# Kernel tuning notes

Hardware: AMD Instinct MI355X
Metric: run time of the kernel (lower is better)

## Reference

```python
import jax, jax.numpy as jnp
import numpy as np
from jax import lax

BN_EPS = 1e-5


def ternarize(w):
    """Per-output-channel ternary quantization (Li & Liu TWN style).
    delta_i = 0.7 * mean(|w_i|); alpha_i = mean of |w| over entries with |w| > delta_i;
    output = alpha_i * (+1 where w > delta_i, -1 where w < -delta_i, else 0).
    """
    aw = jnp.abs(w)
    axes = tuple(range(1, w.ndim))
    delta = 0.7 * jnp.mean(aw, axis=axes)            # [O]
    d = delta.reshape((-1,) + (1,) * (w.ndim - 1))   # broadcastable
    mask = aw > d
    alpha = jnp.sum(aw * mask, axis=axes) / jnp.sum(mask, axis=axes)
    tern = jnp.where(w > d, 1.0, 0.0) - jnp.where(w < -d, 1.0, 0.0)
    return tern * alpha.reshape(d.shape)


def batchnorm2d(x, gamma, beta):
    # training-mode batchnorm: batch statistics over (N, H, W), biased variance
    mean = jnp.mean(x, axis=(0, 2, 3), keepdims=True)
    var = jnp.mean((x - mean) ** 2, axis=(0, 2, 3), keepdims=True)
    xhat = (x - mean) * lax.rsqrt(var + BN_EPS)
    return xhat * gamma[None, :, None, None] + beta[None, :, None, None]


def conv2d(x, w, b):
    out = lax.conv_general_dilated(x, w, window_strides=(1, 1), padding='VALID',
                                   dimension_numbers=('NCHW', 'OIHW', 'NCHW'))
    return out + b[None, :, None, None]


def maxpool2(x):
    return lax.reduce_window(x, -jnp.inf, lax.max, (1, 1, 2, 2), (1, 1, 2, 2), 'VALID')


def setup_inputs() -> dict:
    key = jax.random.key(0)
    ks = jax.random.split(key, 10)
    B = 4096
    return {
        'x': jax.random.normal(ks[0], (B, 1, 28, 28), jnp.float32),
        'w_conv1': jax.random.normal(ks[1], (32, 1, 5, 5), jnp.float32) * 0.2,
        'b_conv1': jax.random.normal(ks[2], (32,), jnp.float32) * 0.1,
        'gamma1': jnp.ones((32,), jnp.float32),
        'beta1': jnp.zeros((32,), jnp.float32),
        'w_conv2': jax.random.normal(ks[3], (64, 32, 5, 5), jnp.float32) * 0.05,
        'b_conv2': jax.random.normal(ks[4], (64,), jnp.float32) * 0.1,
        'gamma2': jnp.ones((64,), jnp.float32),
        'beta2': jnp.zeros((64,), jnp.float32),
        'w_fc1': jax.random.normal(ks[5], (512, 1024), jnp.float32) * 0.03,
        'b_fc1': jax.random.normal(ks[6], (512,), jnp.float32) * 0.1,
        'w_fc2': jax.random.normal(ks[7], (10, 512), jnp.float32) * 0.05,
        'b_fc2': jax.random.normal(ks[8], (10,), jnp.float32) * 0.1,
    }


def reference(x, w_conv1, b_conv1, gamma1, beta1, w_conv2, b_conv2, gamma2, beta2,
              w_fc1, b_fc1, w_fc2, b_fc2):
    h = conv2d(x, ternarize(w_conv1), b_conv1)          # [B,32,24,24]
    h = jax.nn.relu(maxpool2(batchnorm2d(h, gamma1, beta1)))  # [B,32,12,12]
    h = conv2d(h, ternarize(w_conv2), b_conv2)          # [B,64,8,8]
    h = jax.nn.relu(maxpool2(batchnorm2d(h, gamma2, beta2)))  # [B,64,4,4]
    h = h.reshape(-1, 1024)
    h = jax.nn.relu(h @ ternarize(w_fc1).T + b_fc1)     # [B,512]
    return h @ ternarize(w_fc2).T + b_fc2               # [B,10]
```

## Files before the change

### kernel.cpp

```cpp
#include <hip/hip_runtime.h>

#define TID ((int)threadIdx.x)
typedef unsigned short ushort_t;
typedef short short8 __attribute__((ext_vector_type(8)));
typedef float f32x4 __attribute__((ext_vector_type(4)));

__device__ __forceinline__ float bf2f(ushort_t u) {
    return __uint_as_float(((unsigned int)u) << 16);
}
__device__ __forceinline__ ushort_t f2bf(float f) {
    unsigned int x = __float_as_uint(f);
    return (ushort_t)((x + 0x7FFFu + ((x >> 16) & 1u)) >> 16);
}
__device__ __forceinline__ float ld1(const void* p, int i, bool f32) {
    return f32 ? ((const float*)p)[i] : bf2f(((const ushort_t*)p)[i]);
}
__device__ __forceinline__ bool probe_f32(const void* g1) {
    return ((const ushort_t*)g1)[0] == 0x0000u;
}

__global__ __launch_bounds__(256) void tern_pack_kernel(
    const void* __restrict__ w1, const void* __restrict__ w2,
    const void* __restrict__ wf1, const void* __restrict__ wf2,
    ushort_t* __restrict__ wpack1, ushort_t* __restrict__ wpack2,
    ushort_t* __restrict__ wf1pack, ushort_t* __restrict__ wf2pack,
    float* __restrict__ stats_z, const void* __restrict__ g1probe)
{
    const bool f32 = probe_f32(g1probe);
    const int blk = blockIdx.x;
    if (blk < 48) stats_z[blk * 256 + TID] = 0.f;

    const void* w; int K, o, seg;
    if (blk < 32)       { w = w1;  K = 25;   o = blk;       seg = 0; }
    else if (blk < 96)  { w = w2;  K = 800;  o = blk - 32;  seg = 1; }
    else if (blk < 608) { w = wf1; K = 1024; o = blk - 96;  seg = 2; }
    else                { w = wf2; K = 512;  o = blk - 608; seg = 3; }

    const size_t base = (size_t)o * K;
    __shared__ float red[256];
    __shared__ float red2[256];

    float s = 0.f;
    for (int k = TID; k < K; k += 256) s += fabsf(ld1(w, base + k, f32));
    red[TID] = s; __syncthreads();
    for (int st = 128; st > 0; st >>= 1) {
        if (TID < st) red[TID] += red[TID + st];
        __syncthreads();
    }
    const float delta = 0.7f * red[0] / (float)K;
    __syncthreads();

    float ms = 0.f, cnt = 0.f;
    for (int k = TID; k < K; k += 256) {
        float aw = fabsf(ld1(w, base + k, f32));
        if (aw > delta) { ms += aw; cnt += 1.f; }
    }
    red[TID] = ms; red2[TID] = cnt; __syncthreads();
    for (int st = 128; st > 0; st >>= 1) {
        if (TID < st) { red[TID] += red[TID + st]; red2[TID] += red2[TID + st]; }
        __syncthreads();
    }
    const float denom = red2[0];
    const float alpha = (denom > 0.f) ? (red[0] / denom) : 0.f;

    for (int k = TID; k < K; k += 256) {
        float v = ld1(w, base + k, f32);
        ushort_t tb = f2bf((v > delta) ? alpha : ((v < -delta) ? -alpha : 0.f));
        if (seg == 0) {
            const int kp = (k / 5) * 6 + (k % 5);
            wpack1[((size_t)(o >> 4) * 64 + (kp >> 3) * 16 + (o & 15)) * 8 + (kp & 7)] = tb;
        } else if (seg == 1) {
            const int pos = k % 25, ic = k / 25;
            wpack2[((size_t)(pos * 4 + (o >> 4)) * 64 + (ic >> 3) * 16 + (o & 15)) * 8
                   + (ic & 7)] = tb;
        } else if (seg == 2) {
            wf1pack[((size_t)((k >> 5) * 32 + (o >> 4)) * 64 + ((k >> 3) & 3) * 16
                     + (o & 15)) * 8 + (k & 7)] = tb;
        } else {
            wf2pack[((size_t)(k >> 5) * 64 + ((k >> 3) & 3) * 16 + o) * 8 + (k & 7)] = tb;
        }
    }
    if (seg == 0 && TID < 7) {
        const int kps[7] = {5, 11, 17, 23, 29, 30, 31};
        const int kp = kps[TID];
        wpack1[((size_t)(o >> 4) * 64 + (kp >> 3) * 16 + (o & 15)) * 8 + (kp & 7)] = 0;
    }
}

__device__ __forceinline__ void conv1_koff(int qd, int* koff) {
#pragma unroll
    for (int j = 0; j < 8; ++j) {
        int k = qd * 8 + j, ky = k / 6, kx = k - ky * 6;
        koff[j] = (k < 30 && kx < 5) ? (ky * 28 + kx) : -1;
    }
}

__global__ __launch_bounds__(256) void conv1_stats_kernel(
    const void* __restrict__ x, const ushort_t* __restrict__ wpack1u,
    const void* __restrict__ gamma1, float* __restrict__ stats,
    ushort_t* __restrict__ pooled1)
{
    const bool f32 = probe_f32(gamma1);
    const short8* wpack1 = (const short8*)wpack1u;
    __shared__ ushort_t xs[2][784];
    __shared__ float reds[4][64];
    const int b0 = blockIdx.x * 2;
    for (int c = TID; c < 392; c += 256) {
        const int img = (c >= 196) ? 1 : 0;
        const int cc = c - img * 196;
        if (f32) {
            float4 v4 = ((const float4*)x)[(size_t)(b0 + img) * 196 + cc];
            ushort4 u;
            u.x = f2bf(v4.x); u.y = f2bf(v4.y); u.z = f2bf(v4.z); u.w = f2bf(v4.w);
            *(ushort4*)&xs[img][cc * 4] = u;
        } else {
            *(ushort4*)&xs[img][cc * 4] =
                ((const ushort4*)x)[(size_t)(b0 + img) * 196 + cc];
        }
    }
    __syncthreads();

    const int lane = TID & 63, wv = TID >> 6;
    const int img = wv >> 1, wvi = wv & 1;
    const int qd = lane >> 4, ln15 = lane & 15;
    int koff[8];
    conv1_koff(qd, koff);
    const short8 bw0 = wpack1[lane];
    const short8 bw1 = wpack1[64 + lane];
    const bool pos0 = ld1(gamma1, ln15, f32) >= 0.f;
    const bool pos1 = ld1(gamma1, 16 + ln15, f32) >= 0.f;

    float s0 = 0.f, q0 = 0.f, s1 = 0.f, q1 = 0.f;
    const int cellA0 = (ln15 >> 2);
    const int m3 = ln15 & 3;
    const size_t pb = (size_t)(b0 + img) * 144;
    const ushort_t* xsi = xs[img];
    for (int t = wvi * 18; t < wvi * 18 + 18; ++t) {
        const int cellA = t * 4 + cellA0;
        const int pbase = ((cellA / 12) * 2 + (m3 >> 1)) * 28
                        + (cellA % 12) * 2 + (m3 & 1);
        short8 a;
#pragma unroll
        for (int j = 0; j < 8; ++j)
            a[j] = (koff[j] >= 0) ? (short)xsi[pbase + koff[j]] : (short)0;
        f32x4 c0 = {0.f, 0.f, 0.f, 0.f}, c1 = {0.f, 0.f, 0.f, 0.f};
        c0 = __builtin_amdgcn_mfma_f32_16x16x32_bf16(a, bw0, c0, 0, 0, 0);
        c1 = __builtin_amdgcn_mfma_f32_16x16x32_bf16(a, bw1, c1, 0, 0, 0);
#pragma unroll
        for (int r = 0; r < 4; ++r) {
            s0 += c0[r]; q0 += c0[r] * c0[r];
            s1 += c1[r]; q1 += c1[r] * c1[r];
        }
        float mx0 = fmaxf(fmaxf(c0[0], c0[1]), fmaxf(c0[2], c0[3]));
        float mn0 = fminf(fminf(c0[0], c0[1]), fminf(c0[2], c0[3]));
        float mx1 = fmaxf(fmaxf(c1[0], c1[1]), fmaxf(c1[2], c1[3]));
        float mn1 = fminf(fminf(c1[0], c1[1]), fminf(c1[2], c1[3]));
        const int cell = t * 4 + qd;
        pooled1[(pb + cell) * 32 + ln15]      = f2bf(pos0 ? mx0 : mn0);
        pooled1[(pb + cell) * 32 + 16 + ln15] = f2bf(pos1 ? mx1 : mn1);
    }
    s0 += __shfl_xor(s0, 16); q0 += __shfl_xor(q0, 16);
    s1 += __shfl_xor(s1, 16); q1 += __shfl_xor(q1, 16);
    s0 += __shfl_xor(s0, 32); q0 += __shfl_xor(q0, 32);
    s1 += __shfl_xor(s1, 32); q1 += __shfl_xor(q1, 32);
    if (lane < 16) {
        reds[wv][ln15]      = s0;
        reds[wv][32 + ln15] = q0;
        reds[wv][16 + ln15] = s1;
        reds[wv][48 + ln15] = q1;
    }
    __syncthreads();
    if (TID < 64) {
        float v = reds[0][TID] + reds[1][TID] + reds[2][TID] + reds[3][TID];
        atomicAdd(&stats[(blockIdx.x & 63) * 64 + TID], v);
    }
}

__global__ __launch_bounds__(256) void conv12_kernel(
    const ushort_t* __restrict__ pooled1, const float* __restrict__ stats,
    const void* __restrict__ gamma1, const void* __restrict__ beta1,
    const ushort_t* __restrict__ wpack2u,
    const void* __restrict__ b2, const void* __restrict__ gamma2,
    ushort_t* __restrict__ pooled2, float* __restrict__ stats2)
{
    const bool f32 = probe_f32(gamma1);
    const short8* wpack2 = (const short8*)wpack2u;
    __shared__ ushort_t p1b[144 * 40];
    __shared__ float r2[4][64];
    __shared__ float bn4[4][64];
    __shared__ float as1[32], hs1[32];
    const int b = blockIdx.x;

    {
        const int c = TID & 63, g = TID >> 6;
        float v = 0.f;
        for (int sl = g; sl < 64; sl += 4) v += stats[sl * 64 + c];
        bn4[g][c] = v;
    }
    __syncthreads();
    if (TID < 32) {
        float s = bn4[0][TID] + bn4[1][TID] + bn4[2][TID] + bn4[3][TID];
        float q = bn4[0][32 + TID] + bn4[1][32 + TID]
                + bn4[2][32 + TID] + bn4[3][32 + TID];
        const float invN = 1.f / 2359296.f;
        float mraw = s * invN;
        float var  = q * invN - mraw * mraw;
        float rstd = rsqrtf(fmaxf(var, 0.f) + 1e-5f);
        float g1v = ld1(gamma1, TID, f32) * rstd;
        as1[TID] = g1v;
        hs1[TID] = ld1(beta1, TID, f32) - mraw * g1v;
    }
    __syncthreads();

    {
        const uint* pm = (const uint*)(pooled1 + (size_t)b * 4608);
        const int ch2 = (TID * 2) & 31;
        const float aA = as1[ch2],     hA = hs1[ch2];
        const float aB = as1[ch2 + 1], hB = hs1[ch2 + 1];
#pragma unroll
        for (int i = 0; i < 9; ++i) {
            const int idx = i * 256 + TID;
            const uint u = pm[idx];
            const int cell = idx >> 4;
            float v0 = bf2f((ushort_t)(u & 0xFFFFu));
            float v1 = bf2f((ushort_t)(u >> 16));
            uint o0 = f2bf(fmaxf(fmaf(aA, v0, hA), 0.f));
            uint o1 = f2bf(fmaxf(fmaf(aB, v1, hB), 0.f));
            *(uint*)&p1b[cell * 40 + ch2] = o0 | (o1 << 16);
        }
    }
    __syncthreads();

    const int lane = TID & 63, wv = TID >> 6;
    const int qd = lane >> 4, ln15 = lane & 15;
    const int mh = wv >> 1, nh = wv & 1;
    const int px0 = (mh * 2 + 0) * 16 + ln15;
    const int px1 = (mh * 2 + 1) * 16 + ln15;
    const int base0 = (px0 >> 3) * 12 + (px0 & 7);
    const int base1 = (px1 >> 3) * 12 + (px1 & 7);

    f32x4 acc[2][2] = {};
#pragma unroll
    for (int pos = 0; pos < 25; ++pos) {
        const int koff2 = (pos / 5) * 12 + (pos % 5);
        short8 a0 = *(const short8*)&p1b[(base0 + koff2) * 40 + qd * 8];
        short8 a1 = *(const short8*)&p1b[(base1 + koff2) * 40 + qd * 8];
        short8 bb0 = wpack2[(pos * 4 + nh * 2 + 0) * 64 + lane];
        short8 bb1 = wpack2[(pos * 4 + nh * 2 + 1) * 64 + lane];
        acc[0][0] = __builtin_amdgcn_mfma_f32_16x16x32_bf16(a0, bb0, acc[0][0], 0, 0, 0);
        acc[0][1] = __builtin_amdgcn_mfma_f32_16x16x32_bf16(a0, bb1, acc[0][1], 0, 0, 0);
        acc[1][0] = __builtin_amdgcn_mfma_f32_16x16x32_bf16(a1, bb0, acc[1][0], 0, 0, 0);
        acc[1][1] = __builtin_amdgcn_mfma_f32_16x16x32_bf16(a1, bb1, acc[1][1], 0, 0, 0);
    }

    const size_t p2base = (size_t)b * 1024;
#pragma unroll
    for (int jn = 0; jn < 2; ++jn) {
        const int oc = (nh * 2 + jn) * 16 + ln15;
        const float bias = ld1(b2, oc, f32);
        const bool gpos = ld1(gamma2, oc, f32) >= 0.f;
        float s0 = 0.f, q0 = 0.f;
#pragma unroll
        for (int i = 0; i < 2; ++i) {
            float v0 = acc[i][jn][0] + bias;
            float v1 = acc[i][jn][1] + bias;
            float v2 = acc[i][jn][2] + bias;
            float v3 = acc[i][jn][3] + bias;
            s0 += v0 + v1 + v2 + v3;
            q0 += v0*v0 + v1*v1 + v2*v2 + v3*v3;
            float mx01 = fmaxf(v0, v1), mn01 = fminf(v0, v1);
            float mx23 = fmaxf(v2, v3), mn23 = fminf(v2, v3);
            mx01 = fmaxf(mx01, __shfl_xor(mx01, 32));
            mn01 = fminf(mn01, __shfl_xor(mn01, 32));
            mx23 = fmaxf(mx23, __shfl_xor(mx23, 32));
            mn23 = fminf(mn23, __shfl_xor(mn23, 32));
            if (qd < 2) {
                ushort2 st;
                st.x = f2bf(gpos ? mx01 : mn01);
                st.y = f2bf(gpos ? mx23 : mn23);
                const int ti = mh * 2 + i;
                *(ushort2*)&pooled2[p2base + (size_t)oc * 16 + ti * 4 + 2 * qd] = st;
            }
        }
        s0 += __shfl_down(s0, 32); q0 += __shfl_down(q0, 32);
        s0 += __shfl_down(s0, 16); q0 += __shfl_down(q0, 16);
        if (lane < 16) {
            r2[wv][jn * 32 + lane]      = s0;
            r2[wv][jn * 32 + 16 + lane] = q0;
        }
    }
    __syncthreads();
    if (TID < 128) {
        const int idx = TID & 63, nh2 = TID >> 6;
        float v = r2[nh2][idx] + r2[nh2 + 2][idx];
        const int jn = idx >> 5, isq = (idx >> 4) & 1, chx = idx & 15;
        const int oc = nh2 * 32 + jn * 16 + chx;
        atomicAdd(&stats2[(blockIdx.x & 63) * 128 + isq * 64 + oc], v);
    }
}

__global__ __launch_bounds__(256) void fc1_kernel(
    const ushort_t* __restrict__ pooled2, const ushort_t* __restrict__ wf1packu,
    const float* __restrict__ stats2,
    const void* __restrict__ gamma2, const void* __restrict__ beta2,
    const void* __restrict__ bias, ushort_t* __restrict__ out,
    const void* __restrict__ g1probe)
{
    const bool f32 = probe_f32(g1probe);
    const short8* wf1pack = (const short8*)wf1packu;
    __shared__ ushort_t As[64 * 136];
    __shared__ float bn2[2][128];
    __shared__ float a2s[64], h2s[64];
    const int m0 = blockIdx.y * 64;
    const int n0x4 = blockIdx.x * 4;
    const int lane = TID & 63;
    const int wv   = TID >> 6;
    const int mh = wv >> 1, nh = wv & 1;
    const int qd = lane >> 4, ln15 = lane & 15;

    {
        const int c = TID & 127, g = TID >> 7;
        float v = 0.f;
        for (int sl = g; sl < 64; sl += 2) v += stats2[sl * 128 + c];
        bn2[g][c] = v;
    }
    __syncthreads();
    if (TID < 64) {
        float s = bn2[0][TID] + bn2[1][TID];
        float q = bn2[0][64 + TID] + bn2[1][64 + TID];
        const float invN = 1.f / 262144.f;
        float mean = s * invN;
        float var  = q * invN - mean * mean;
        float rstd = rsqrtf(fmaxf(var, 0.f) + 1e-5f);
        float g2 = ld1(gamma2, TID, f32) * rstd;
        a2s[TID] = g2;
        h2s[TID] = ld1(beta2, TID, f32) - mean * g2;
    }

    f32x4 acc[2][2] = {};
    for (int stage = 0; stage < 8; ++stage) {
        __syncthreads();
#pragma unroll
        for (int i = 0; i < 4; ++i) {
            const int idx = i * 256 + TID;
            const int row = idx >> 4, ch = idx & 15;
            const int k = stage * 128 + ch * 8;
            const int oc = k >> 4;
            const float a2 = a2s[oc], h2 = h2s[oc];
            uint4 u = *(const uint4*)&pooled2[(size_t)(m0 + row) * 1024 + k];
            uint4 o;
            uint* up = &u.x; uint* op = &o.x;
#pragma unroll
            for (int q = 0; q < 4; ++q) {
                float lo = bf2f((ushort_t)(up[q] & 0xFFFFu));
                float hi = bf2f((ushort_t)(up[q] >> 16));
                uint olo = f2bf(fmaxf(fmaf(a2, lo, h2), 0.f));
                uint ohi = f2bf(fmaxf(fmaf(a2, hi, h2), 0.f));
                op[q] = olo | (ohi << 16);
            }
            *(uint4*)&As[row * 136 + ch * 8] = o;
        }
        __syncthreads();
#pragma unroll
        for (int ks = 0; ks < 4; ++ks) {
            const int kk = stage * 4 + ks;
            const int col = ks * 32 + qd * 8;
            short8 a0 = *(const short8*)&As[(mh * 32 + ln15) * 136 + col];
            short8 a1 = *(const short8*)&As[(mh * 32 + 16 + ln15) * 136 + col];
            short8 bb0 = wf1pack[(kk * 32 + n0x4 + nh * 2 + 0) * 64 + lane];
            short8 bb1 = wf1pack[(kk * 32 + n0x4 + nh * 2 + 1) * 64 + lane];
            acc[0][0] = __builtin_amdgcn_mfma_f32_16x16x32_bf16(a0, bb0, acc[0][0], 0, 0, 0);
            acc[0][1] = __builtin_amdgcn_mfma_f32_16x16x32_bf16(a0, bb1, acc[0][1], 0, 0, 0);
            acc[1][0] = __builtin_amdgcn_mfma_f32_16x16x32_bf16(a1, bb0, acc[1][0], 0, 0, 0);
            acc[1][1] = __builtin_amdgcn_mfma_f32_16x16x32_bf16(a1, bb1, acc[1][1], 0, 0, 0);
        }
    }

#pragma unroll
    for (int jn = 0; jn < 2; ++jn) {
        const int n = n0x4 * 16 + (nh * 2 + jn) * 16 + ln15;
        const float bv = ld1(bias, n, f32);
#pragma unroll
        for (int i = 0; i < 2; ++i) {
            const int mb = m0 + (mh * 2 + i) * 16 + qd * 4;
#pragma unroll
            for (int r = 0; r < 4; ++r) {
                float v = fmaxf(acc[i][jn][r] + bv, 0.f);
                out[(size_t)(mb + r) * 512 + n] = f2bf(v);
            }
        }
    }
}

__global__ __launch_bounds__(256) void fc2_kernel(
    const ushort_t* __restrict__ h, const ushort_t* __restrict__ wf2packu,
    const void* __restrict__ bias, void* __restrict__ out,
    const void* __restrict__ g1probe)
{
    const bool f32 = probe_f32(g1probe);
    const short8* wf2pack = (const short8*)wf2packu;
    const int lane = TID & 63, wv = TID >> 6;
    const int qd = lane >> 4, ln15 = lane & 15;
    const int m0 = (blockIdx.x * 4 + wv) * 16;

    f32x4 acc = {0.f, 0.f, 0.f, 0.f};
#pragma unroll
    for (int kk = 0; kk < 16; ++kk) {
        short8 a = *(const short8*)&h[(size_t)(m0 + ln15) * 512 + kk * 32 + qd * 8];
        acc = __builtin_amdgcn_mfma_f32_16x16x32_bf16(a, wf2pack[kk * 64 + lane],
                                                      acc, 0, 0, 0);
    }
    if (ln15 < 10) {
        const float bv = ld1(bias, ln15, f32);
#pragma unroll
        for (int r = 0; r < 4; ++r) {
            const size_t oi = (size_t)(m0 + qd * 4 + r) * 10 + ln15;
            float v = acc[r] + bv;
            if (f32) ((float*)out)[oi] = v;
            else ((ushort_t*)out)[oi] = f2bf(v);
        }
    }
}

extern "C" void kernel_launch(void* const* d_in, const int* in_sizes, int n_in,
                              void* d_out, int out_size, void* d_ws, size_t ws_size,
                              hipStream_t stream)
{
    const void* x       = d_in[0];
    const void* w_conv1 = d_in[1];
    const void* b_conv1 = d_in[2];
    const void* gamma1  = d_in[3];
    const void* beta1   = d_in[4];
    const void* w_conv2 = d_in[5];
    const void* b_conv2 = d_in[6];
    const void* gamma2  = d_in[7];
    const void* beta2   = d_in[8];
    const void* w_fc1   = d_in[9];
    const void* b_fc1   = d_in[10];
    const void* w_fc2   = d_in[11];
    const void* b_fc2   = d_in[12];
    (void)b_conv1;

    char* wsb = (char*)d_ws;
    size_t off = 0;
    auto alloc = [&](size_t bytes) -> void* {
        void* p = wsb + off;
        off += (bytes + 255) & ~(size_t)255;
        return p;
    };

    float*    stats   = (float*)alloc(49152);
    float*    stats2  = stats + 4096;
    ushort_t* wpack1  = (ushort_t*)alloc(2 * 64 * 16);
    ushort_t* wpack2  = (ushort_t*)alloc(25 * 4 * 64 * 16);
    ushort_t* wf1pack = (ushort_t*)alloc((size_t)32 * 32 * 64 * 16);
    ushort_t* wf2pack = (ushort_t*)alloc(16 * 64 * 16);
    ushort_t* pooled1 = (ushort_t*)alloc((size_t)4096 * 144 * 32 * 2);
    ushort_t* pooled2 = (ushort_t*)alloc((size_t)4096 * 64 * 16 * 2);
    ushort_t* fc1o    = (ushort_t*)alloc((size_t)4096 * 512 * 2);

    tern_pack_kernel<<<618, 256, 0, stream>>>(w_conv1, w_conv2, w_fc1, w_fc2,
                                              wpack1, wpack2, wf1pack, wf2pack,
                                              stats, gamma1);

    conv1_stats_kernel<<<2048, 256, 0, stream>>>(x, wpack1, gamma1, stats, pooled1);

    conv12_kernel<<<4096, 256, 0, stream>>>(pooled1, stats, gamma1, beta1,
                                            wpack2, b_conv2, gamma2,
                                            pooled2, stats2);

    fc1_kernel<<<dim3(8, 64), 256, 0, stream>>>(pooled2, wf1pack, stats2,
                                                gamma2, beta2, b_fc1, fc1o, gamma1);
    fc2_kernel<<<64, 256, 0, stream>>>(fc1o, wf2pack, b_fc2, d_out, gamma1);
}
```

Baseline: 192.0 us.

## Finalize BN stats in last block and apply BN2 in separate pass

Each of conv1 and conv12 now finishes with a completion counter: the last block to arrive sums the 64 partial-stat slices and writes per-channel BN scale and shift. Downstream blocks then read 32 or 64 ready values instead of every block re-reducing all slices. BN2+ReLU moves into a standalone elementwise kernel that updates pooled2 in place, so fc1 loads A fragments straight from global memory without an LDS staging pass or barriers. The cost is an extra kernel launch plus a full read and write of pooled2, atomic counters and fences at the end of every block, and uncoalesced direct A loads in fc1.

```diff
diff --git a/kernel.cpp b/kernel.cpp
--- a/kernel.cpp
+++ b/kernel.cpp
@@ -14,6 +14,9 @@
 }
 __device__ __forceinline__ float ld1(const void* p, int i, bool f32) {
     return f32 ? ((const float*)p)[i] : bf2f(((const ushort_t*)p)[i]);
+}
+__device__ __forceinline__ float aload(const float* p) {
+    return __hip_atomic_load(p, __ATOMIC_RELAXED, __HIP_MEMORY_SCOPE_AGENT);
 }
 __device__ __forceinline__ bool probe_f32(const void* g1) {
     return ((const ushort_t*)g1)[0] == 0x0000u;
@@ -28,7 +31,7 @@
 {
     const bool f32 = probe_f32(g1probe);
     const int blk = blockIdx.x;
-    if (blk < 48) stats_z[blk * 256 + TID] = 0.f;
+    if (blk < 49) stats_z[blk * 256 + TID] = 0.f;
 
     const void* w; int K, o, seg;
     if (blk < 32)       { w = w1;  K = 25;   o = blk;       seg = 0; }
@@ -97,13 +100,16 @@
 
 __global__ __launch_bounds__(256) void conv1_stats_kernel(
     const void* __restrict__ x, const ushort_t* __restrict__ wpack1u,
-    const void* __restrict__ gamma1, float* __restrict__ stats,
-    ushort_t* __restrict__ pooled1)
+    const void* __restrict__ gamma1, const void* __restrict__ beta1,
+    float* __restrict__ stats, ushort_t* __restrict__ pooled1,
+    float* __restrict__ sc1, float* __restrict__ sh1,
+    unsigned int* __restrict__ ctr)
 {
     const bool f32 = probe_f32(gamma1);
     const short8* wpack1 = (const short8*)wpack1u;
     __shared__ ushort_t xs[2][784];
     __shared__ float reds[4][64];
+    __shared__ unsigned int islast;
     const int b0 = blockIdx.x * 2;
     for (int c = TID; c < 392; c += 256) {
         const int img = (c >= 196) ? 1 : 0;
@@ -174,42 +180,48 @@
         float v = reds[0][TID] + reds[1][TID] + reds[2][TID] + reds[3][TID];
         atomicAdd(&stats[(blockIdx.x & 63) * 64 + TID], v);
     }
+
+    __threadfence();
+    __syncthreads();
+    if (TID == 0) islast = (atomicAdd(ctr, 1u) == 2047u) ? 1u : 0u;
+    __syncthreads();
+    if (islast) {
+        if (TID < 64) {
+            float v = 0.f;
+            for (int sl = 0; sl < 64; ++sl) v += aload(&stats[sl * 64 + TID]);
+            reds[0][TID] = v;
+        }
+        __syncthreads();
+        if (TID < 32) {
+            const float invN = 1.f / 2359296.f;
+            float mraw = reds[0][TID] * invN;
+            float var  = reds[0][32 + TID] * invN - mraw * mraw;
+            float rstd = rsqrtf(fmaxf(var, 0.f) + 1e-5f);
+            float g = ld1(gamma1, TID, f32) * rstd;
+            sc1[TID] = g;
+            sh1[TID] = ld1(beta1, TID, f32) - mraw * g;
+        }
+    }
 }
 
 __global__ __launch_bounds__(256) void conv12_kernel(
-    const ushort_t* __restrict__ pooled1, const float* __restrict__ stats,
-    const void* __restrict__ gamma1, const void* __restrict__ beta1,
+    const ushort_t* __restrict__ pooled1,
+    const float* __restrict__ sc1, const float* __restrict__ sh1,
     const ushort_t* __restrict__ wpack2u,
     const void* __restrict__ b2, const void* __restrict__ gamma2,
-    ushort_t* __restrict__ pooled2, float* __restrict__ stats2)
-{
-    const bool f32 = probe_f32(gamma1);
+    const void* __restrict__ beta2,
+    ushort_t* __restrict__ pooled2, float* __restrict__ stats2,
+    float* __restrict__ sc2, float* __restrict__ sh2,
+    unsigned int* __restrict__ ctr, const void* __restrict__ g1probe)
+{
+    const bool f32 = probe_f32(g1probe);
     const short8* wpack2 = (const short8*)wpack2u;
     __shared__ ushort_t p1b[144 * 40];
     __shared__ float r2[4][64];
-    __shared__ float bn4[4][64];
     __shared__ float as1[32], hs1[32];
+    __shared__ unsigned int islast;
     const int b = blockIdx.x;
-
-    {
-        const int c = TID & 63, g = TID >> 6;
-        float v = 0.f;
-        for (int sl = g; sl < 64; sl += 4) v += stats[sl * 64 + c];
-        bn4[g][c] = v;
-    }
-    __syncthreads();
-    if (TID < 32) {
-        float s = bn4[0][TID] + bn4[1][TID] + bn4[2][TID] + bn4[3][TID];
-        float q = bn4[0][32 + TID] + bn4[1][32 + TID]
-                + bn4[2][32 + TID] + bn4[3][32 + TID];
-        const float invN = 1.f / 2359296.f;
-        float mraw = s * invN;
-        float var  = q * invN - mraw * mraw;
-        float rstd = rsqrtf(fmaxf(var, 0.f) + 1e-5f);
-        float g1v = ld1(gamma1, TID, f32) * rstd;
-        as1[TID] = g1v;
-        hs1[TID] = ld1(beta1, TID, f32) - mraw * g1v;
-    }
+    if (TID < 32) { as1[TID] = sc1[TID]; hs1[TID] = sh1[TID]; }
     __syncthreads();
 
     {
@@ -297,83 +309,78 @@
         const int oc = nh2 * 32 + jn * 16 + chx;
         atomicAdd(&stats2[(blockIdx.x & 63) * 128 + isq * 64 + oc], v);
     }
+
+    __threadfence();
+    __syncthreads();
+    if (TID == 0) islast = (atomicAdd(ctr, 1u) == 4095u) ? 1u : 0u;
+    __syncthreads();
+    if (islast) {
+        float* flat = &r2[0][0];
+        if (TID < 128) {
+            float v = 0.f;
+            for (int sl = 0; sl < 64; ++sl) v += aload(&stats2[sl * 128 + TID]);
+            flat[TID] = v;
+        }
+        __syncthreads();
+        if (TID < 64) {
+            const float invN = 1.f / 262144.f;
+            float mean = flat[TID] * invN;
+            float var  = flat[64 + TID] * invN - mean * mean;
+            float rstd = rsqrtf(fmaxf(var, 0.f) + 1e-5f);
+            float g2 = ld1(gamma2, TID, f32) * rstd;
+            sc2[TID] = g2;
+            sh2[TID] = ld1(beta2, TID, f32) - mean * g2;
+        }
+    }
+}
+
+__global__ __launch_bounds__(256) void bn2relu_kernel(
+    ushort_t* __restrict__ pooled2,
+    const float* __restrict__ sc2, const float* __restrict__ sh2)
+{
+    const int idx = blockIdx.x * 256 + TID;
+    const int r = idx & 127;
+    const float a = sc2[r >> 1], h = sh2[r >> 1];
+    uint4 u = ((uint4*)pooled2)[idx];
+    uint* up = &u.x;
+#pragma unroll
+    for (int q = 0; q < 4; ++q) {
+        float lo = bf2f((ushort_t)(up[q] & 0xFFFFu));
+        float hi = bf2f((ushort_t)(up[q] >> 16));
+        uint olo = f2bf(fmaxf(fmaf(a, lo, h), 0.f));
+        uint ohi = f2bf(fmaxf(fmaf(a, hi, h), 0.f));
+        up[q] = olo | (ohi << 16);
+    }
+    ((uint4*)pooled2)[idx] = u;
 }
 
 __global__ __launch_bounds__(256) void fc1_kernel(
-    const ushort_t* __restrict__ pooled2, const ushort_t* __restrict__ wf1packu,
-    const float* __restrict__ stats2,
-    const void* __restrict__ gamma2, const void* __restrict__ beta2,
+    const ushort_t* __restrict__ A, const ushort_t* __restrict__ wf1packu,
     const void* __restrict__ bias, ushort_t* __restrict__ out,
     const void* __restrict__ g1probe)
 {
     const bool f32 = probe_f32(g1probe);
     const short8* wf1pack = (const short8*)wf1packu;
-    __shared__ ushort_t As[64 * 136];
-    __shared__ float bn2[2][128];
-    __shared__ float a2s[64], h2s[64];
     const int m0 = blockIdx.y * 64;
     const int n0x4 = blockIdx.x * 4;
     const int lane = TID & 63;
     const int wv   = TID >> 6;
     const int mh = wv >> 1, nh = wv & 1;
     const int qd = lane >> 4, ln15 = lane & 15;
-
-    {
-        const int c = TID & 127, g = TID >> 7;
-        float v = 0.f;
-        for (int sl = g; sl < 64; sl += 2) v += stats2[sl * 128 + c];
-        bn2[g][c] = v;
-    }
-    __syncthreads();
-    if (TID < 64) {
-        float s = bn2[0][TID] + bn2[1][TID];
-        float q = bn2[0][64 + TID] + bn2[1][64 + TID];
-        const float invN = 1.f / 262144.f;
-        float mean = s * invN;
-        float var  = q * invN - mean * mean;
-        float rstd = rsqrtf(fmaxf(var, 0.f) + 1e-5f);
-        float g2 = ld1(gamma2, TID, f32) * rstd;
-        a2s[TID] = g2;
-        h2s[TID] = ld1(beta2, TID, f32) - mean * g2;
-    }
+    const ushort_t* arow0 = A + (size_t)(m0 + mh * 32 + ln15) * 1024 + qd * 8;
+    const ushort_t* arow1 = arow0 + 16 * 1024;
 
     f32x4 acc[2][2] = {};
-    for (int stage = 0; stage < 8; ++stage) {
-        __syncthreads();
-#pragma unroll
-        for (int i = 0; i < 4; ++i) {
-            const int idx = i * 256 + TID;
-            const int row = idx >> 4, ch = idx & 15;
-            const int k = stage * 128 + ch * 8;
-            const int oc = k >> 4;
-            const float a2 = a2s[oc], h2 = h2s[oc];
-            uint4 u = *(const uint4*)&pooled2[(size_t)(m0 + row) * 1024 + k];
-            uint4 o;
-            uint* up = &u.x; uint* op = &o.x;
-#pragma unroll
-            for (int q = 0; q < 4; ++q) {
-                float lo = bf2f((ushort_t)(up[q] & 0xFFFFu));
-                float hi = bf2f((ushort_t)(up[q] >> 16));
-                uint olo = f2bf(fmaxf(fmaf(a2, lo, h2), 0.f));
-                uint ohi = f2bf(fmaxf(fmaf(a2, hi, h2), 0.f));
-                op[q] = olo | (ohi << 16);
-            }
-            *(uint4*)&As[row * 136 + ch * 8] = o;
-        }
-        __syncthreads();
-#pragma unroll
-        for (int ks = 0; ks < 4; ++ks) {
-            const int kk = stage * 4 + ks;
-            const int col = ks * 32 + qd * 8;
-            short8 a0 = *(const short8*)&As[(mh * 32 + ln15) * 136 + col];
-            short8 a1 = *(const short8*)&As[(mh * 32 + 16 + ln15) * 136 + col];
-            short8 bb0 = wf1pack[(kk * 32 + n0x4 + nh * 2 + 0) * 64 + lane];
-            short8 bb1 = wf1pack[(kk * 32 + n0x4 + nh * 2 + 1) * 64 + lane];
-            acc[0][0] = __builtin_amdgcn_mfma_f32_16x16x32_bf16(a0, bb0, acc[0][0], 0, 0, 0);
-            acc[0][1] = __builtin_amdgcn_mfma_f32_16x16x32_bf16(a0, bb1, acc[0][1], 0, 0, 0);
-            acc[1][0] = __builtin_amdgcn_mfma_f32_16x16x32_bf16(a1, bb0, acc[1][0], 0, 0, 0);
-            acc[1][1] = __builtin_amdgcn_mfma_f32_16x16x32_bf16(a1, bb1, acc[1][1], 0, 0, 0);
-        }
+#pragma unroll 8
+    for (int kk = 0; kk < 32; ++kk) {
+        short8 a0 = *(const short8*)(arow0 + kk * 32);
+        short8 a1 = *(const short8*)(arow1 + kk * 32);
+        short8 bb0 = wf1pack[(kk * 32 + n0x4 + nh * 2 + 0) * 64 + lane];
+        short8 bb1 = wf1pack[(kk * 32 + n0x4 + nh * 2 + 1) * 64 + lane];
+        acc[0][0] = __builtin_amdgcn_mfma_f32_16x16x32_bf16(a0, bb0, acc[0][0], 0, 0, 0);
+        acc[0][1] = __builtin_amdgcn_mfma_f32_16x16x32_bf16(a0, bb1, acc[0][1], 0, 0, 0);
+        acc[1][0] = __builtin_amdgcn_mfma_f32_16x16x32_bf16(a1, bb0, acc[1][0], 0, 0, 0);
+        acc[1][1] = __builtin_amdgcn_mfma_f32_16x16x32_bf16(a1, bb1, acc[1][1], 0, 0, 0);
     }
 
 #pragma unroll
@@ -428,7 +435,6 @@
 {
     const void* x       = d_in[0];
     const void* w_conv1 = d_in[1];
-    const void* b_conv1 = d_in[2];
     const void* gamma1  = d_in[3];
     const void* beta1   = d_in[4];
     const void* w_conv2 = d_in[5];
@@ -439,7 +445,6 @@
     const void* b_fc1   = d_in[10];
     const void* w_fc2   = d_in[11];
     const void* b_fc2   = d_in[12];
-    (void)b_conv1;
 
     char* wsb = (char*)d_ws;
     size_t off = 0;
@@ -449,8 +454,13 @@
         return p;
     };
 
-    float*    stats   = (float*)alloc(49152);
+    float*    stats   = (float*)alloc(50176);
     float*    stats2  = stats + 4096;
+    unsigned int* ctrs = (unsigned int*)(stats + 12288);
+    float*    sc1     = (float*)alloc(128);
+    float*    sh1     = (float*)alloc(128);
+    float*    sc2     = (float*)alloc(256);
+    float*    sh2     = (float*)alloc(256);
     ushort_t* wpack1  = (ushort_t*)alloc(2 * 64 * 16);
     ushort_t* wpack2  = (ushort_t*)alloc(25 * 4 * 64 * 16);
     ushort_t* wf1pack = (ushort_t*)alloc((size_t)32 * 32 * 64 * 16);
@@ -463,13 +473,17 @@
                                               wpack1, wpack2, wf1pack, wf2pack,
                                               stats, gamma1);
 
-    conv1_stats_kernel<<<2048, 256, 0, stream>>>(x, wpack1, gamma1, stats, pooled1);
-
-    conv12_kernel<<<4096, 256, 0, stream>>>(pooled1, stats, gamma1, beta1,
-                                            wpack2, b_conv2, gamma2,
-                                            pooled2, stats2);
-
-    fc1_kernel<<<dim3(8, 64), 256, 0, stream>>>(pooled2, wf1pack, stats2,
-                                                gamma2, beta2, b_fc1, fc1o, gamma1);
+    conv1_stats_kernel<<<2048, 256, 0, stream>>>(x, wpack1, gamma1, beta1,
+                                                 stats, pooled1, sc1, sh1, ctrs);
+
+    conv12_kernel<<<4096, 256, 0, stream>>>(pooled1, sc1, sh1, wpack2,
+                                            b_conv2, gamma2, beta2,
+                                            pooled2, stats2, sc2, sh2,
+                                            ctrs + 1, gamma1);
+
+    bn2relu_kernel<<<2048, 256, 0, stream>>>(pooled2, sc2, sh2);
+
+    fc1_kernel<<<dim3(8, 64), 256, 0, stream>>>(pooled2, wf1pack, b_fc1,
+                                                fc1o, gamma1);
     fc2_kernel<<<64, 256, 0, stream>>>(fc1o, wf2pack, b_fc2, d_out, gamma1);
 }
```

Result: slower. 757.7 us (+294.6%).
